# Optimization experiments

Hardware: AMD Instinct MI355X
Metric: run time of the kernel (lower is better)

The kernel has to match this reference:

```python
import jax, jax.numpy as jnp
import numpy as np

L = 4          # dilation_depth
HID = 32       # hidden_channels
F_IN = 16
F_OUT = 16
K = 2          # conv kernel size


def setup_inputs() -> dict:
    key = jax.random.key(0)
    ks = jax.random.split(key, 20)
    B, T, N, F = 8, 512, 128, F_IN
    s = 0.1
    inp = {
        "X": jax.random.normal(ks[0], (B, T, N, F), jnp.float32),
        "A": jax.random.normal(ks[1], (N, N), jnp.float32) / jnp.sqrt(N).astype(jnp.float32),
        "in_w": jax.random.normal(ks[2], (F, 3 * HID), jnp.float32) * s,
        "in_b": jnp.zeros((3 * HID,), jnp.float32),
        "ct_w": jax.random.normal(ks[3], (L, K, HID, HID), jnp.float32) * s,
        "ct_b": jnp.zeros((L, HID), jnp.float32),
        "cs_w": jax.random.normal(ks[4], (L, K, HID, HID), jnp.float32) * s,
        "cs_b": jnp.zeros((L, HID), jnp.float32),
        "gcn_w": jax.random.normal(ks[5], (L, HID, HID), jnp.float32) * s,
        "gcn_b": jnp.zeros((L, HID), jnp.float32),
        "res_w": jax.random.normal(ks[6], (L, HID, HID), jnp.float32) * s,
        "res_b": jnp.zeros((L, HID), jnp.float32),
        "skip_w": jax.random.normal(ks[7], (L, HID, HID), jnp.float32) * s,
        "skip_b": jnp.zeros((L, HID), jnp.float32),
        "out1_w": jax.random.normal(ks[8], (HID, HID), jnp.float32) * s,
        "out1_b": jnp.zeros((HID,), jnp.float32),
        "out2_w": jax.random.normal(ks[9], (HID, F_OUT), jnp.float32) * s,
        "out2_b": jnp.zeros((F_OUT,), jnp.float32),
    }
    return inp


def _causal_conv(x, w, b, dilation):
    # x: [BN, T, C]; w: [K, C_in, C_out] (WIO); causal pad left by dilation*(K-1)
    pad = dilation * (w.shape[0] - 1)
    y = jax.lax.conv_general_dilated(
        x, w, window_strides=(1,), padding=[(pad, 0)],
        rhs_dilation=(dilation,), dimension_numbers=("NWC", "WIO", "NWC"))
    return y + b


def reference(X, A, in_w, in_b, ct_w, ct_b, cs_w, cs_b, gcn_w, gcn_b,
              res_w, res_b, skip_w, skip_b, out1_w, out1_b, out2_w, out2_b):
    B, T, N, F = X.shape
    Xp = X @ in_w + in_b                      # [B,T,N,3H]
    x_a, x_b, x_res = jnp.split(Xp, 3, axis=-1)
    H = x_a.shape[-1]
    # Faithful to source: raw reshape [B,T,N,H] -> [B*N,T,H] (no transpose), as in the original code.
    x_a_r = x_a.reshape(B * N, T, H)
    x_b_r = x_b.reshape(B * N, T, H)
    skip = jnp.zeros_like(x_res)
    for i in range(L):
        d = 2 ** i
        tcn = (jnp.tanh(_causal_conv(x_a_r, ct_w[i], ct_b[i], d))
               * jax.nn.sigmoid(_causal_conv(x_b_r, cs_w[i], cs_b[i], d)))
        tcn = tcn.reshape(B, N, T, H).transpose(0, 2, 1, 3)   # [B,T,N,H]
        gcn = jnp.einsum('ij,btjf->btif', A, x_res) @ gcn_w[i] + gcn_b[i]
        h = tcn + gcn
        x_res = (h @ res_w[i] + res_b[i]) + x_res
        skip = skip + (h @ skip_w[i] + skip_b[i])
    h = jax.nn.relu(skip)
    h = jax.nn.relu(h @ out1_w + out1_b)
    return h @ out2_w + out2_b
```

## Files before the change

kernel.cpp:

```cpp
#include <hip/hip_runtime.h>
#include <math.h>

#define T_ 512

typedef _Float16 half8 __attribute__((ext_vector_type(8)));
typedef _Float16 half4 __attribute__((ext_vector_type(4)));
typedef float f32x4 __attribute__((ext_vector_type(4)));

__device__ __forceinline__ float ts_act(float a, float b) {
    float e2a = __expf(a + a);
    float eb  = __expf(b);
    float num = (e2a - 1.0f) * eb;
    float den = (e2a + 1.0f) * (eb + 1.0f);
    return num * __builtin_amdgcn_rcpf(den);
}

__device__ __forceinline__ half4 pack4(f32x4 v) {
    half4 h;
    h[0] = (_Float16)v[0]; h[1] = (_Float16)v[1];
    h[2] = (_Float16)v[2]; h[3] = (_Float16)v[3];
    return h;
}

__global__ __launch_bounds__(256) void k_prep(
    const float* __restrict__ A,     const float* __restrict__ in_w,
    const float* __restrict__ in_b,
    const float* __restrict__ ct_w,  const float* __restrict__ ct_b,
    const float* __restrict__ cs_w,  const float* __restrict__ cs_b,
    const float* __restrict__ gcn_w, const float* __restrict__ res_w,
    const float* __restrict__ skip_w,
    const float* __restrict__ out1_w,const float* __restrict__ out2_w,
    _Float16* __restrict__ FR, float* __restrict__ BIAS)
{
    int idx = blockIdx.x * 256 + threadIdx.x;
    if (idx < 16384) {
        int j = idx & 7, L = (idx >> 3) & 63, tile = idx >> 9;
        int it = tile >> 2, kt = tile & 3;
        FR[idx] = (_Float16)A[(it * 16 + (L & 15)) * 128 + kt * 32 + (L >> 4) * 8 + j];
    } else if (idx < 24576) {
        int e = idx - 16384;
        int j = e & 7, L = (e >> 3) & 63, ct = (e >> 9) & 1, mat = e >> 10;
        int k = (L >> 4) * 8 + j, col = ct * 16 + (L & 15);
        int l = mat >> 1, br = mat & 1;
        const float* tw = (br ? cs_w : ct_w) + l * 2048;
        int bro = br * 32;
        float v = 0.f;
        if (k < 16) { for (int c = 0; c < 32; ++c) v += in_w[k*96 + bro + c] * tw[c*32 + col]; }
        else        { for (int c = 0; c < 32; ++c) v += in_w[(k-16)*96 + bro + c] * tw[1024 + c*32 + col]; }
        FR[idx] = (_Float16)v;
    } else if (idx < 39936) {
        int e = idx - 24576;
        int i = e & 3, L = (e >> 2) & 63, ct = (e >> 8) & 1, ks = (e >> 9) & 1, mat = e >> 10;
        int k = ks * 16 + (L >> 4) * 4 + i, col = ct * 16 + (L & 15);
        float v;
        if (mat < 12) {
            int l = mat / 3, r = mat - l * 3;
            const float* W = (r == 0) ? gcn_w : (r == 1) ? res_w : skip_w;
            v = W[l * 1024 + k * 32 + col];
        } else if (mat == 12) v = out1_w[k * 32 + col];
        else if (mat == 13)   v = (ct == 0) ? out2_w[k * 16 + (L & 15)] : 0.f;
        else                  v = (ks == 0) ? in_w[k * 96 + 64 + col] : 0.f;
        FR[idx] = (_Float16)v;
    } else if (idx < 40448) {
        int e = idx - 39936;
        int n = e & 31, br = (e >> 5) & 1, pvi = (e >> 6) & 1, l = e >> 7;
        const float* W  = br ? cs_w : ct_w;
        const float* bb = br ? cs_b : ct_b;
        int ibo = br * 32;
        float v = bb[l * 32 + n];
        for (int c = 0; c < 32; ++c) v += in_b[ibo + c] * W[l*2048 + 1024 + c*32 + n];
        if (pvi)
            for (int c = 0; c < 32; ++c) v += in_b[ibo + c] * W[l*2048 + c*32 + n];
        BIAS[e] = v;
    }
}

__global__ __launch_bounds__(256, 3) void k_fused(
    const float* __restrict__ X,
    const _Float16* __restrict__ FR,
    const float* __restrict__ BIAS,
    const float* __restrict__ in_b,
    const float* __restrict__ gcn_b,
    const float* __restrict__ res_b,
    const float* __restrict__ skip_b,
    const float* __restrict__ b1,
    const float* __restrict__ b2,
    float* __restrict__ out)
{
    __shared__ _Float16 Pld[128 * 88];
    __shared__ _Float16 xsT[2][32 * 136];

    const int bx = blockIdx.x;
    const int btid = ((bx & 7) << 9) | (bx >> 3);
    const int b = btid >> 9, t = btid & (T_ - 1);
    const int tid = threadIdx.x, lane = tid & 63, w = tid >> 6;
    const int lm = lane & 15, kb = lane >> 4;
    const int R = w * 32;
    const int row = lane >> 1, ch = lane & 1;

    const half8* AFv  = (const half8*)FR;
    const half8* W32v = (const half8*)(FR + 16384);
    const half4* W16v = (const half4*)(FR + 24576);
    const f32x4 zero4 = {0.f, 0.f, 0.f, 0.f};

    {
        const size_t nrow = (size_t)(b * 128 + R + row) * T_;
        const float4* xc = (const float4*)(X + (nrow + t) * 16 + ch * 8);
        float4 c0 = xc[0], c1 = xc[1];
        float4 p0[4], p1[4];
#pragma unroll
        for (int l = 0; l < 4; ++l) {
            const int d = 1 << l;
            if (t >= d) {
                const float4* xp = (const float4*)(X + (nrow + (t - d)) * 16 + ch * 8);
                p0[l] = xp[0]; p1[l] = xp[1];
            } else {
                p0[l] = make_float4(0.f, 0.f, 0.f, 0.f);
                p1[l] = make_float4(0.f, 0.f, 0.f, 0.f);
            }
        }
        half8 hv;
        hv[0]=(_Float16)c0.x; hv[1]=(_Float16)c0.y; hv[2]=(_Float16)c0.z; hv[3]=(_Float16)c0.w;
        hv[4]=(_Float16)c1.x; hv[5]=(_Float16)c1.y; hv[6]=(_Float16)c1.z; hv[7]=(_Float16)c1.w;
        *(half8*)&Pld[(R + row) * 88 + 64 + ch * 8] = hv;
#pragma unroll
        for (int l = 0; l < 4; ++l) {
            hv[0]=(_Float16)p0[l].x; hv[1]=(_Float16)p0[l].y; hv[2]=(_Float16)p0[l].z; hv[3]=(_Float16)p0[l].w;
            hv[4]=(_Float16)p1[l].x; hv[5]=(_Float16)p1[l].y; hv[6]=(_Float16)p1[l].z; hv[7]=(_Float16)p1[l].w;
            *(half8*)&Pld[(R + row) * 88 + l * 16 + ch * 8] = hv;
        }
    }

    f32x4 xm[2][2], skT[2][2];
    {
        const float4 x0 = *(const float4*)(X + ((size_t)btid * 128 + R + lm) * 16 + kb * 4);
        const float4 x1 = *(const float4*)(X + ((size_t)btid * 128 + R + 16 + lm) * 16 + kb * 4);
        half4 p0, p1;
        p0[0]=(_Float16)x0.x; p0[1]=(_Float16)x0.y; p0[2]=(_Float16)x0.z; p0[3]=(_Float16)x0.w;
        p1[0]=(_Float16)x1.x; p1[1]=(_Float16)x1.y; p1[2]=(_Float16)x1.z; p1[3]=(_Float16)x1.w;
#pragma unroll
        for (int f = 0; f < 2; ++f) {
            half4 wi = W16v[(56 + f) * 64 + lane];
            float bi = in_b[64 + f * 16 + lm];
            f32x4 cb; cb[0] = bi; cb[1] = bi; cb[2] = bi; cb[3] = bi;
            xm[0][f] = __builtin_amdgcn_mfma_f32_16x16x16f16(p0, wi, cb, 0, 0, 0);
            xm[1][f] = __builtin_amdgcn_mfma_f32_16x16x16f16(p1, wi, cb, 0, 0, 0);
        }
#pragma unroll
        for (int f3 = 0; f3 < 2; ++f3) {
            f32x4 s = zero4;
#pragma unroll
            for (int l = 0; l < 4; ++l) {
                const float4 q = *(const float4*)&skip_b[l * 32 + f3 * 16 + kb * 4];
                s[0] += q.x; s[1] += q.y; s[2] += q.z; s[3] += q.w;
            }
            skT[f3][0] = s; skT[f3][1] = s;
        }
    }

    const int fragoff = (kb < 2) ? kb * 8 : 64 + (kb - 2) * 8;
    const int lstep   = (kb < 2) ? 16 : 0;

#pragma unroll 1
    for (int l = 0; l < 4; ++l) {
        const bool pv = (t >= (1 << l));
        const float* B2 = BIAS + (l * 2 + (pv ? 1 : 0)) * 64;
        const int buf = l & 1;

#pragma unroll
        for (int mt = 0; mt < 2; ++mt)
#pragma unroll
            for (int f = 0; f < 2; ++f)
                *(half4*)&xsT[buf][(f * 16 + lm) * 136 + R + mt * 16 + kb * 4] = pack4(xm[mt][f]);

        half8 Afr[2][4];
#pragma unroll
        for (int mt = 0; mt < 2; ++mt)
#pragma unroll
            for (int kt = 0; kt < 4; ++kt)
                Afr[mt][kt] = AFv[((w * 2 + mt) * 4 + kt) * 64 + lane];
        const f32x4 cT0 = *(const f32x4*)&B2[0 * 16 + kb * 4];
        const f32x4 cT1 = *(const f32x4*)&B2[1 * 16 + kb * 4];
        const f32x4 cS0 = *(const f32x4*)&B2[32 + 0 * 16 + kb * 4];
        const f32x4 cS1 = *(const f32x4*)&B2[32 + 1 * 16 + kb * 4];

        __syncthreads();

        const int poff = fragoff + l * lstep;
        half8 pf0 = *(const half8*)&Pld[(R + lm) * 88 + poff];
        half8 pf1 = *(const half8*)&Pld[(R + 16 + lm) * 88 + poff];
        f32x4 dt[2][2], ds[2][2];
#pragma unroll
        for (int ct = 0; ct < 2; ++ct) {
            half8 wt = W32v[((l * 2 + 0) * 2 + ct) * 64 + lane];
            half8 ws = W32v[((l * 2 + 1) * 2 + ct) * 64 + lane];
            const f32x4 cT = ct ? cT1 : cT0;
            const f32x4 cS = ct ? cS1 : cS0;
            dt[ct][0] = __builtin_amdgcn_mfma_f32_16x16x32_f16(wt, pf0, cT, 0, 0, 0);
            dt[ct][1] = __builtin_amdgcn_mfma_f32_16x16x32_f16(wt, pf1, cT, 0, 0, 0);
            ds[ct][0] = __builtin_amdgcn_mfma_f32_16x16x32_f16(ws, pf0, cS, 0, 0, 0);
            ds[ct][1] = __builtin_amdgcn_mfma_f32_16x16x32_f16(ws, pf1, cS, 0, 0, 0);
        }

        f32x4 AxT[2][2];
#pragma unroll
        for (int f = 0; f < 2; ++f) {
            half8 xa[4];
#pragma unroll
            for (int kt = 0; kt < 4; ++kt)
                xa[kt] = *(const half8*)&xsT[buf][(f * 16 + lm) * 136 + kt * 32 + kb * 8];
#pragma unroll
            for (int mt = 0; mt < 2; ++mt) {
                f32x4 acc = zero4;
#pragma unroll
                for (int kt = 0; kt < 4; ++kt)
                    acc = __builtin_amdgcn_mfma_f32_16x16x32_f16(xa[kt], Afr[mt][kt], acc, 0, 0, 0);
                AxT[f][mt] = acc;
            }
        }

        f32x4 tcv[2][2];
#pragma unroll
        for (int ct = 0; ct < 2; ++ct)
#pragma unroll
            for (int mt = 0; mt < 2; ++mt)
#pragma unroll
                for (int r = 0; r < 4; ++r)
                    tcv[ct][mt][r] = ts_act(dt[ct][mt][r], ds[ct][mt][r]);

        half4 axh[2][2];
#pragma unroll
        for (int f = 0; f < 2; ++f)
#pragma unroll
            for (int mt = 0; mt < 2; ++mt) axh[f][mt] = pack4(AxT[f][mt]);
        half4 hh[2][2];
#pragma unroll
        for (int g = 0; g < 2; ++g) {
            half4 gw0 = W16v[((l * 3 + 0) * 4 + 0 + g) * 64 + lane];
            half4 gw1 = W16v[((l * 3 + 0) * 4 + 2 + g) * 64 + lane];
            const f32x4 gq = *(const f32x4*)&gcn_b[l * 32 + g * 16 + kb * 4];
#pragma unroll
            for (int mt = 0; mt < 2; ++mt) {
                f32x4 acc = __builtin_amdgcn_mfma_f32_16x16x16f16(gw0, axh[0][mt], gq, 0, 0, 0);
                acc = __builtin_amdgcn_mfma_f32_16x16x16f16(gw1, axh[1][mt], acc, 0, 0, 0);
#pragma unroll
                for (int r = 0; r < 4; ++r) acc[r] += tcv[g][mt][r];
                hh[g][mt] = pack4(acc);
            }
        }

#pragma unroll
        for (int mt = 0; mt < 2; ++mt)
#pragma unroll
            for (int f3 = 0; f3 < 2; ++f3) {
                half4 rw0 = W16v[((l * 3 + 1) * 4 + 0 + f3) * 64 + lane];
                half4 rw1 = W16v[((l * 3 + 1) * 4 + 2 + f3) * 64 + lane];
                f32x4 acc = __builtin_amdgcn_mfma_f32_16x16x16f16(hh[0][mt], rw0, xm[mt][f3], 0, 0, 0);
                xm[mt][f3] = __builtin_amdgcn_mfma_f32_16x16x16f16(hh[1][mt], rw1, acc, 0, 0, 0);
                float rb = res_b[l * 32 + f3 * 16 + lm];
#pragma unroll
                for (int r = 0; r < 4; ++r) xm[mt][f3][r] += rb;

                half4 sw0 = W16v[((l * 3 + 2) * 4 + 0 + f3) * 64 + lane];
                half4 sw1 = W16v[((l * 3 + 2) * 4 + 2 + f3) * 64 + lane];
                f32x4 acs = __builtin_amdgcn_mfma_f32_16x16x16f16(sw0, hh[0][mt], skT[f3][mt], 0, 0, 0);
                skT[f3][mt] = __builtin_amdgcn_mfma_f32_16x16x16f16(sw1, hh[1][mt], acs, 0, 0, 0);
            }
    }

    half4 rs[2][2];
#pragma unroll
    for (int g = 0; g < 2; ++g)
#pragma unroll
        for (int mt = 0; mt < 2; ++mt) {
            f32x4 v;
#pragma unroll
            for (int r = 0; r < 4; ++r) v[r] = fmaxf(skT[g][mt][r], 0.f);
            rs[g][mt] = pack4(v);
        }
    half4 h1h[2][2];
#pragma unroll
    for (int g4 = 0; g4 < 2; ++g4) {
        half4 w10 = W16v[(48 + 0 + g4) * 64 + lane];
        half4 w11 = W16v[(48 + 2 + g4) * 64 + lane];
        const f32x4 bq = *(const f32x4*)&b1[g4 * 16 + kb * 4];
#pragma unroll
        for (int mt = 0; mt < 2; ++mt) {
            f32x4 acc = __builtin_amdgcn_mfma_f32_16x16x16f16(w10, rs[0][mt], bq, 0, 0, 0);
            acc = __builtin_amdgcn_mfma_f32_16x16x16f16(w11, rs[1][mt], acc, 0, 0, 0);
            f32x4 v;
#pragma unroll
            for (int r = 0; r < 4; ++r) v[r] = fmaxf(acc[r], 0.f);
            h1h[g4][mt] = pack4(v);
        }
    }
    {
        half4 w20 = W16v[(52 + 0) * 64 + lane];
        half4 w21 = W16v[(52 + 2) * 64 + lane];
        const f32x4 b2q = *(const f32x4*)&b2[kb * 4];
#pragma unroll
        for (int mt = 0; mt < 2; ++mt) {
            f32x4 acc = __builtin_amdgcn_mfma_f32_16x16x16f16(w20, h1h[0][mt], b2q, 0, 0, 0);
            acc = __builtin_amdgcn_mfma_f32_16x16x16f16(w21, h1h[1][mt], acc, 0, 0, 0);
            float4 o = make_float4(acc[0], acc[1], acc[2], acc[3]);
            *(float4*)&out[((size_t)btid * 128 + R + mt * 16 + lm) * 16 + kb * 4] = o;
        }
    }
}

extern "C" void kernel_launch(void* const* d_in, const int* in_sizes, int n_in,
                              void* d_out, int out_size, void* d_ws, size_t ws_size,
                              hipStream_t stream)
{
    const float* X      = (const float*)d_in[0];
    const float* A      = (const float*)d_in[1];
    const float* in_w   = (const float*)d_in[2];
    const float* in_b   = (const float*)d_in[3];
    const float* ct_w   = (const float*)d_in[4];
    const float* ct_b   = (const float*)d_in[5];
    const float* cs_w   = (const float*)d_in[6];
    const float* cs_b   = (const float*)d_in[7];
    const float* gcn_w  = (const float*)d_in[8];
    const float* gcn_b  = (const float*)d_in[9];
    const float* res_w  = (const float*)d_in[10];
    const float* res_b  = (const float*)d_in[11];
    const float* skip_w = (const float*)d_in[12];
    const float* skip_b = (const float*)d_in[13];
    const float* out1_w = (const float*)d_in[14];
    const float* out1_b = (const float*)d_in[15];
    const float* out2_w = (const float*)d_in[16];
    const float* out2_b = (const float*)d_in[17];

    _Float16* FR   = (_Float16*)d_ws;
    float*    BIAS = (float*)((char*)d_ws + 79872);

    k_prep<<<158, 256, 0, stream>>>(A, in_w, in_b, ct_w, ct_b, cs_w, cs_b,
                                    gcn_w, res_w, skip_w, out1_w, out2_w,
                                    FR, BIAS);

    k_fused<<<8 * T_, 256, 0, stream>>>(X, FR, BIAS, in_b,
                                        gcn_b, res_b, skip_b,
                                        out1_b, out2_b, (float*)d_out);
}
```

Baseline: 195.6 us.

## Prescale conv weights by log2e, use exp2, packed cvt, hoist A frags, unroll layers

Folds the log2(e) factors for tanh and sigmoid into the precomputed conv weights and biases so the gate uses raw exp2. It also switches fp32-to-fp16 conversion to packed round-toward-zero instructions, hoists the adjacency fragment loads out of the layer loop, and fully unrolls the four-layer loop. The gate output now seeds the GCN MFMA accumulator together with the GCN bias, which removes the separate adds. Risks are more register pressure from the hoisted fragments and the unrolled loop under launch bounds (256,3), and small rounding differences from RTZ conversion and fp16-scaled weights.

```diff
diff --git a/kernel.cpp b/kernel.cpp
--- a/kernel.cpp
+++ b/kernel.cpp
@@ -5,20 +5,43 @@
 
 typedef _Float16 half8 __attribute__((ext_vector_type(8)));
 typedef _Float16 half4 __attribute__((ext_vector_type(4)));
+typedef _Float16 half2 __attribute__((ext_vector_type(2)));
+typedef __fp16  pk2   __attribute__((ext_vector_type(2)));
 typedef float f32x4 __attribute__((ext_vector_type(4)));
 
-__device__ __forceinline__ float ts_act(float a, float b) {
-    float e2a = __expf(a + a);
-    float eb  = __expf(b);
+__device__ __forceinline__ half2 cvt2(float x, float y) {
+    pk2 p = __builtin_amdgcn_cvt_pkrtz(x, y);
+    return __builtin_bit_cast(half2, p);
+}
+
+__device__ __forceinline__ float ts_act2(float a, float b, float gb) {
+    float e2a = __builtin_exp2f(a);
+    float eb  = __builtin_exp2f(b);
     float num = (e2a - 1.0f) * eb;
     float den = (e2a + 1.0f) * (eb + 1.0f);
-    return num * __builtin_amdgcn_rcpf(den);
+    return fmaf(num, __builtin_amdgcn_rcpf(den), gb);
 }
 
 __device__ __forceinline__ half4 pack4(f32x4 v) {
-    half4 h;
-    h[0] = (_Float16)v[0]; h[1] = (_Float16)v[1];
-    h[2] = (_Float16)v[2]; h[3] = (_Float16)v[3];
+    half2 lo = cvt2(v[0], v[1]);
+    half2 hi = cvt2(v[2], v[3]);
+    half4 h; h[0] = lo[0]; h[1] = lo[1]; h[2] = hi[0]; h[3] = hi[1];
+    return h;
+}
+__device__ __forceinline__ half4 pack4f(float4 v) {
+    half2 lo = cvt2(v.x, v.y);
+    half2 hi = cvt2(v.z, v.w);
+    half4 h; h[0] = lo[0]; h[1] = lo[1]; h[2] = hi[0]; h[3] = hi[1];
+    return h;
+}
+__device__ __forceinline__ half8 pack8(float4 u0, float4 u1) {
+    half2 a = cvt2(u0.x, u0.y);
+    half2 b = cvt2(u0.z, u0.w);
+    half2 c = cvt2(u1.x, u1.y);
+    half2 d = cvt2(u1.z, u1.w);
+    half8 h;
+    h[0]=a[0]; h[1]=a[1]; h[2]=b[0]; h[3]=b[1];
+    h[4]=c[0]; h[5]=c[1]; h[6]=d[0]; h[7]=d[1];
     return h;
 }
 
@@ -47,6 +70,7 @@
         float v = 0.f;
         if (k < 16) { for (int c = 0; c < 32; ++c) v += in_w[k*96 + bro + c] * tw[c*32 + col]; }
         else        { for (int c = 0; c < 32; ++c) v += in_w[(k-16)*96 + bro + c] * tw[1024 + c*32 + col]; }
+        v *= (br ? 1.4426950408889634f : 2.8853900817779268f);
         FR[idx] = (_Float16)v;
     } else if (idx < 39936) {
         int e = idx - 24576;
@@ -71,7 +95,7 @@
         for (int c = 0; c < 32; ++c) v += in_b[ibo + c] * W[l*2048 + 1024 + c*32 + n];
         if (pvi)
             for (int c = 0; c < 32; ++c) v += in_b[ibo + c] * W[l*2048 + c*32 + n];
-        BIAS[e] = v;
+        BIAS[e] = v * (br ? 1.4426950408889634f : 2.8853900817779268f);
     }
 }
 
@@ -119,25 +143,24 @@
                 p1[l] = make_float4(0.f, 0.f, 0.f, 0.f);
             }
         }
-        half8 hv;
-        hv[0]=(_Float16)c0.x; hv[1]=(_Float16)c0.y; hv[2]=(_Float16)c0.z; hv[3]=(_Float16)c0.w;
-        hv[4]=(_Float16)c1.x; hv[5]=(_Float16)c1.y; hv[6]=(_Float16)c1.z; hv[7]=(_Float16)c1.w;
-        *(half8*)&Pld[(R + row) * 88 + 64 + ch * 8] = hv;
-#pragma unroll
-        for (int l = 0; l < 4; ++l) {
-            hv[0]=(_Float16)p0[l].x; hv[1]=(_Float16)p0[l].y; hv[2]=(_Float16)p0[l].z; hv[3]=(_Float16)p0[l].w;
-            hv[4]=(_Float16)p1[l].x; hv[5]=(_Float16)p1[l].y; hv[6]=(_Float16)p1[l].z; hv[7]=(_Float16)p1[l].w;
-            *(half8*)&Pld[(R + row) * 88 + l * 16 + ch * 8] = hv;
-        }
-    }
+        *(half8*)&Pld[(R + row) * 88 + 64 + ch * 8] = pack8(c0, c1);
+#pragma unroll
+        for (int l = 0; l < 4; ++l)
+            *(half8*)&Pld[(R + row) * 88 + l * 16 + ch * 8] = pack8(p0[l], p1[l]);
+    }
+
+    half8 Afr[2][4];
+#pragma unroll
+    for (int mt = 0; mt < 2; ++mt)
+#pragma unroll
+        for (int kt = 0; kt < 4; ++kt)
+            Afr[mt][kt] = AFv[((w * 2 + mt) * 4 + kt) * 64 + lane];
 
     f32x4 xm[2][2], skT[2][2];
     {
         const float4 x0 = *(const float4*)(X + ((size_t)btid * 128 + R + lm) * 16 + kb * 4);
         const float4 x1 = *(const float4*)(X + ((size_t)btid * 128 + R + 16 + lm) * 16 + kb * 4);
-        half4 p0, p1;
-        p0[0]=(_Float16)x0.x; p0[1]=(_Float16)x0.y; p0[2]=(_Float16)x0.z; p0[3]=(_Float16)x0.w;
-        p1[0]=(_Float16)x1.x; p1[1]=(_Float16)x1.y; p1[2]=(_Float16)x1.z; p1[3]=(_Float16)x1.w;
+        half4 p0 = pack4f(x0), p1 = pack4f(x1);
 #pragma unroll
         for (int f = 0; f < 2; ++f) {
             half4 wi = W16v[(56 + f) * 64 + lane];
@@ -161,7 +184,7 @@
     const int fragoff = (kb < 2) ? kb * 8 : 64 + (kb - 2) * 8;
     const int lstep   = (kb < 2) ? 16 : 0;
 
-#pragma unroll 1
+#pragma unroll
     for (int l = 0; l < 4; ++l) {
         const bool pv = (t >= (1 << l));
         const float* B2 = BIAS + (l * 2 + (pv ? 1 : 0)) * 64;
@@ -173,16 +196,12 @@
             for (int f = 0; f < 2; ++f)
                 *(half4*)&xsT[buf][(f * 16 + lm) * 136 + R + mt * 16 + kb * 4] = pack4(xm[mt][f]);
 
-        half8 Afr[2][4];
-#pragma unroll
-        for (int mt = 0; mt < 2; ++mt)
-#pragma unroll
-            for (int kt = 0; kt < 4; ++kt)
-                Afr[mt][kt] = AFv[((w * 2 + mt) * 4 + kt) * 64 + lane];
         const f32x4 cT0 = *(const f32x4*)&B2[0 * 16 + kb * 4];
         const f32x4 cT1 = *(const f32x4*)&B2[1 * 16 + kb * 4];
         const f32x4 cS0 = *(const f32x4*)&B2[32 + 0 * 16 + kb * 4];
         const f32x4 cS1 = *(const f32x4*)&B2[32 + 1 * 16 + kb * 4];
+        const f32x4 gq0 = *(const f32x4*)&gcn_b[l * 32 + 0 * 16 + kb * 4];
+        const f32x4 gq1 = *(const f32x4*)&gcn_b[l * 32 + 1 * 16 + kb * 4];
 
         __syncthreads();
 
@@ -221,12 +240,14 @@
 
         f32x4 tcv[2][2];
 #pragma unroll
-        for (int ct = 0; ct < 2; ++ct)
+        for (int ct = 0; ct < 2; ++ct) {
+            const f32x4 gq = ct ? gq1 : gq0;
 #pragma unroll
             for (int mt = 0; mt < 2; ++mt)
 #pragma unroll
                 for (int r = 0; r < 4; ++r)
-                    tcv[ct][mt][r] = ts_act(dt[ct][mt][r], ds[ct][mt][r]);
+                    tcv[ct][mt][r] = ts_act2(dt[ct][mt][r], ds[ct][mt][r], gq[r]);
+        }
 
         half4 axh[2][2];
 #pragma unroll
@@ -238,13 +259,10 @@
         for (int g = 0; g < 2; ++g) {
             half4 gw0 = W16v[((l * 3 + 0) * 4 + 0 + g) * 64 + lane];
             half4 gw1 = W16v[((l * 3 + 0) * 4 + 2 + g) * 64 + lane];
-            const f32x4 gq = *(const f32x4*)&gcn_b[l * 32 + g * 16 + kb * 4];
 #pragma unroll
             for (int mt = 0; mt < 2; ++mt) {
-                f32x4 acc = __builtin_amdgcn_mfma_f32_16x16x16f16(gw0, axh[0][mt], gq, 0, 0, 0);
-                acc = __builtin_amdgcn_mfma_f32_16x16x16f16(gw1, axh[1][mt], acc, 0, 0, 0);
-#pragma unroll
-                for (int r = 0; r < 4; ++r) acc[r] += tcv[g][mt][r];
+                f32x4 acc = __builtin_amdgcn_mfma_f32_16x16x16f16(gw1, axh[1][mt], tcv[g][mt], 0, 0, 0);
+                acc = __builtin_amdgcn_mfma_f32_16x16x16f16(gw0, axh[0][mt], acc, 0, 0, 0);
                 hh[g][mt] = pack4(acc);
             }
         }
```

Measured after the change: 209.2 us. 7.0% more time.
